# Kernel tuning notes

Measured on AMD Instinct MI355X. Metric: run time of the kernel, lower is better.

## Reference

```python
import jax, jax.numpy as jnp
import numpy as np

HEADS = 8
EPS_LN = 1e-5
EPS_N = 1e-12


def _dw(x, w, b, pad):
    # depthwise conv, NCHW, weight [C,1,kh,kw]
    C = x.shape[1]
    y = jax.lax.conv_general_dilated(x, w, (1, 1), pad,
                                     dimension_numbers=('NCHW', 'OIHW', 'NCHW'),
                                     feature_group_count=C)
    return y + b[None, :, None, None]


def _pw(x, w, b):
    # 1x1 conv as einsum, weight [Cout, Cin]
    return jnp.einsum('bihw,oi->bohw', x, w) + b[None, :, None, None]


def _l2n(x):
    n = jnp.sqrt(jnp.sum(x * x, axis=-1, keepdims=True))
    return x / jnp.maximum(n, EPS_N)


def _axis_attn(q, k, v):
    # q,k,v: [B, heads, N, D]; L2-normalized QK, softmax, +q residual
    q = _l2n(q)
    k = _l2n(k)
    attn = jax.nn.softmax(jnp.einsum('bhnd,bhmd->bhnm', q, k), axis=-1)
    return jnp.einsum('bhnm,bhmd->bhnd', attn, v) + q


def setup_inputs() -> dict:
    key = jax.random.key(0)
    B, C, H, W = 16, 256, 80, 80
    ks = jax.random.split(key, 16)

    def nrm(k, shape, s=0.02):
        return jax.random.normal(k, shape, dtype=jnp.float32) * s

    z = lambda *s: jnp.zeros(s, jnp.float32)
    return {
        'x': nrm(ks[0], (B, C, H, W), 1.0),
        'ln_g': jnp.ones((C,), jnp.float32),
        'ln_b': z(C),
        'w_in': nrm(ks[1], (C, C)), 'b_in': z(C),
        'w_out': nrm(ks[2], (C, C)), 'b_out': z(C),
        'wx7': nrm(ks[3], (C, 1, 1, 7)), 'bx7': z(C),
        'wx11': nrm(ks[4], (C, 1, 1, 11)), 'bx11': z(C),
        'wx21': nrm(ks[5], (C, 1, 1, 21)), 'bx21': z(C),
        'wy7': nrm(ks[6], (C, 1, 7, 1)), 'by7': z(C),
        'wy11': nrm(ks[7], (C, 1, 11, 1)), 'by11': z(C),
        'wy21': nrm(ks[8], (C, 1, 21, 1)), 'by21': z(C),
    }


def reference(x, ln_g, ln_b, w_in, b_in, w_out, b_out,
              wx7, bx7, wx11, bx11, wx21, bx21,
              wy7, by7, wy11, by11, wy21, by21):
    B, C, H, W = x.shape
    cp = C // HEADS

    # LayerNorm over channel dim (applied per-pixel)
    mu = jnp.mean(x, axis=1, keepdims=True)
    var = jnp.var(x, axis=1, keepdims=True)
    xn = (x - mu) / jnp.sqrt(var + EPS_LN)
    xn = xn * ln_g[None, :, None, None] + ln_b[None, :, None, None]

    fx = _pw(_dw(xn, wx7, bx7, ((0, 0), (3, 3)))
             + _dw(xn, wx11, bx11, ((0, 0), (5, 5)))
             + _dw(xn, wx21, bx21, ((0, 0), (10, 10))), w_in, b_in)
    fy = _pw(_dw(xn, wy7, by7, ((3, 3), (0, 0)))
             + _dw(xn, wy11, by11, ((5, 5), (0, 0)))
             + _dw(xn, wy21, by21, ((10, 10), (0, 0))), w_in, b_in)

    def to_h(t):  # [B,C,H,W] -> [B,heads,H,W*cp] (w outer, c inner)
        return t.reshape(B, HEADS, cp, H, W).transpose(0, 1, 3, 4, 2).reshape(B, HEADS, H, W * cp)

    def from_h(t):
        return t.reshape(B, HEADS, H, W, cp).transpose(0, 1, 4, 2, 3).reshape(B, C, H, W)

    def to_w(t):  # [B,C,H,W] -> [B,heads,W,H*cp] (h outer, c inner)
        return t.reshape(B, HEADS, cp, H, W).transpose(0, 1, 4, 3, 2).reshape(B, HEADS, W, H * cp)

    def from_w(t):
        return t.reshape(B, HEADS, W, H, cp).transpose(0, 1, 4, 3, 2).reshape(B, C, H, W)

    out_x = from_h(_axis_attn(to_h(fy), to_h(fx), to_h(fx)))
    out_y = from_w(_axis_attn(to_w(fx), to_w(fy), to_w(fy)))

    return _pw(out_x, w_out, b_out) + _pw(out_y, w_out, b_out) + x
```

## Files before the change

kernel.cpp:

```cpp
#include <hip/hip_runtime.h>

typedef unsigned short u16;
typedef unsigned int   u32;

#define NB  16
#define NC  256
#define NH  80
#define NW  80
#define NHW 6400

typedef short bf16x8 __attribute__((ext_vector_type(8)));
typedef float f32x4  __attribute__((ext_vector_type(4)));

__device__ __forceinline__ float b2f(u16 u) {
  union { u32 i; float f; } c; c.i = ((u32)u) << 16; return c.f;
}
__device__ __forceinline__ u16 f2b(float f) {
  union { float f; u32 i; } c; c.f = f;
  return (u16)((c.i + 0x7FFFu + ((c.i >> 16) & 1u)) >> 16);
}
__device__ __forceinline__ float ldx(const void* p, size_t i, int f32f) {
  return f32f ? ((const float*)p)[i] : b2f(((const u16*)p)[i]);
}
__device__ __forceinline__ int getf(int fh, const int* flagp) {
  return (fh >= 0) ? fh : *flagp;
}

__global__ void probe_init(int* __restrict__ flag) { flag[0] = 0; flag[1] = 0; }

__global__ __launch_bounds__(256) void probe_count(const u16* __restrict__ x,
                                                   int* __restrict__ flag)
{
  __shared__ int cnt[256];
  int base = (blockIdx.x * 256 + threadIdx.x) * 16;
  int c = 0;
  uint4 v0 = *(const uint4*)(x + base);
  uint4 v1 = *(const uint4*)(x + base + 8);
  u32 w[8] = {v0.x, v0.y, v0.z, v0.w, v1.x, v1.y, v1.z, v1.w};
  #pragma unroll
  for (int j = 0; j < 8; j++) {
    if (((w[j] >> 7)  & 0xFFu) == 0xFFu) c++;
    if (((w[j] >> 23) & 0xFFu) == 0xFFu) c++;
  }
  cnt[threadIdx.x] = c; __syncthreads();
  for (int s = 128; s > 0; s >>= 1) {
    if (threadIdx.x < s) cnt[threadIdx.x] += cnt[threadIdx.x + s];
    __syncthreads();
  }
  if (threadIdx.x == 0) atomicAdd(&flag[1], cnt[0]);
}

__global__ void probe_decide(int* __restrict__ flag) {
  flag[0] = (flag[1] > 16) ? 1 : 0;
}

struct CvtArgs { const void* src[18]; int cum[19]; };

__global__ __launch_bounds__(256) void cvt_weights(CvtArgs a, float* __restrict__ dst,
                                                   int fh, const int* __restrict__ flagp)
{
  int f = getf(fh, flagp);
  int i = blockIdx.x * 256 + threadIdx.x;
  int s = 0;
  while (i >= a.cum[s + 1]) s++;
  int j = i - a.cum[s];
  float v = f ? ((const float*)a.src[s])[j] : b2f(((const u16*)a.src[s])[j]);
  if (!(v == v) || fabsf(v) > 1e30f) v = 0.f;
  dst[i] = v;
}

__global__ __launch_bounds__(256) void split_w(const float* __restrict__ w_in,
    const float* __restrict__ w_out, u16* __restrict__ WB)
{
  int i = blockIdx.x * 256 + threadIdx.x;
  int mat = i >> 16, idx = i & 65535;
  float v = (mat ? w_out : w_in)[idx];
  u16 hi = f2b(v);
  u16 lo = f2b(v - b2f(hi));
  WB[mat * 131072 + idx] = hi;
  WB[mat * 131072 + 65536 + idx] = lo;
}

__global__ __launch_bounds__(256) void ln_stats(const void* __restrict__ xsrc,
    size_t xoff, int fh, const int* __restrict__ flagp, float2* __restrict__ stats)
{
  int f = getf(fh, flagp);
  int p = blockIdx.x * 256 + threadIdx.x;
  int bl = p / NHW, hw = p % NHW;
  size_t base = xoff + (size_t)bl * NC * NHW + hw;
  float s1 = 0.f, s2 = 0.f;
  for (int c = 0; c < NC; c++) {
    float v = ldx(xsrc, base + (size_t)c * NHW, f);
    s1 += v; s2 += v * v;
  }
  float mean = s1 * (1.f / 256.f);
  float var  = s2 * (1.f / 256.f) - mean * mean;
  stats[p] = make_float2(mean, rsqrtf(var + 1e-5f));
}

__global__ __launch_bounds__(256) void dw_both(const void* __restrict__ xsrc,
    size_t xoff, int fh, const int* __restrict__ flagp,
    const float2* __restrict__ stats,
    const float* __restrict__ g, const float* __restrict__ bt,
    const float* __restrict__ wx7,  const float* __restrict__ bx7,
    const float* __restrict__ wx11, const float* __restrict__ bx11,
    const float* __restrict__ wx21, const float* __restrict__ bx21,
    const float* __restrict__ wy7,  const float* __restrict__ by7,
    const float* __restrict__ wy11, const float* __restrict__ by11,
    const float* __restrict__ wy21, const float* __restrict__ by21,
    u16* __restrict__ sx, u16* __restrict__ sy)
{
  __shared__ float xn[80][81];
  __shared__ float cwx[21], cwy[21];
  __shared__ float cbx, cby;
  int f = getf(fh, flagp);
  int bc = blockIdx.x;
  int c  = bc & 255;
  int bl = bc >> 8;
  int t = threadIdx.x;
  if (t < 21) {
    float v = wx21[c * 21 + t];
    if (t >= 5 && t <= 15) v += wx11[c * 11 + t - 5];
    if (t >= 7 && t <= 13) v += wx7[c * 7 + t - 7];
    cwx[t] = v;
  } else if (t < 42) {
    int j = t - 21;
    float v = wy21[c * 21 + j];
    if (j >= 5 && j <= 15) v += wy11[c * 11 + j - 5];
    if (j >= 7 && j <= 13) v += wy7[c * 7 + j - 7];
    cwy[j] = v;
  } else if (t == 42) { cbx = bx7[c] + bx11[c] + bx21[c]; }
  else if (t == 43)   { cby = by7[c] + by11[c] + by21[c]; }
  float cg = g[c], cbt = bt[c];
  size_t xrow = xoff + (size_t)bc * NHW;
  const float2* st = stats + (size_t)bl * NHW;
  for (int i = t; i < NHW; i += 256) {
    float v = ldx(xsrc, xrow + i, f);
    float2 s = st[i];
    xn[i / 80][i % 80] = (v - s.x) * s.y * cg + cbt;
  }
  __syncthreads();
  float bxv = cbx, byv = cby;
  size_t obase = (size_t)bc * NHW;
  for (int k = 0; k < 25; k++) {
    int p = t + 256 * k;
    int h = p / 80, w = p % 80;
    float ax = bxv, ay = byv;
    #pragma unroll
    for (int d = -10; d <= 10; d++) {
      int wp = w + d;
      if (wp >= 0 && wp < NW) ax += cwx[d + 10] * xn[h][wp];
      int hp = h + d;
      if (hp >= 0 && hp < NH) ay += cwy[d + 10] * xn[hp][w];
    }
    sx[obase + p] = f2b(ax);
    sy[obase + p] = f2b(ay);
  }
}

template<int FINAL>
__global__ __launch_bounds__(256) void pw_mfma_t(const u16* __restrict__ WB,
    u16* io0, u16* io1, const float* __restrict__ bias,
    void* __restrict__ OutBase, size_t out_off,
    const void* __restrict__ xsrc, size_t xoff,
    int fh, const int* __restrict__ flagp)
{
  __shared__ u16 S[32768];
  u16* InT = S;
  u16* Wp  = S + 16384;
  int bl = blockIdx.y;
  int p0 = blockIdx.x * 64;
  int t  = threadIdx.x;
  int lane = t & 63, wid = t >> 6, lg = lane >> 4, lr = lane & 15;
  u16* io = (FINAL || blockIdx.z == 0) ? io0 : io1;

  {
    int kb = t >> 3, pb = t & 7;
    const u16* src = io + (size_t)bl * NC * NHW + p0 + pb * 8;
    u32 r[8][4];
    #pragma unroll
    for (int i = 0; i < 8; i++) {
      uint4 v = *(const uint4*)(src + (size_t)(kb * 8 + i) * NHW);
      r[i][0] = v.x; r[i][1] = v.y; r[i][2] = v.z; r[i][3] = v.w;
    }
    #pragma unroll
    for (int j = 0; j < 8; j++) {
      u32 w[4];
      #pragma unroll
      for (int m = 0; m < 4; m++) {
        u32 a = r[2 * m][j >> 1], b = r[2 * m + 1][j >> 1];
        w[m] = (j & 1) ? ((a >> 16) | (b & 0xFFFF0000u))
                       : ((a & 0xFFFFu) | (b << 16));
      }
      int p = pb * 8 + j;
      *(uint4*)&InT[p * 256 + ((kb ^ j) * 8)] = make_uint4(w[0], w[1], w[2], w[3]);
    }
  }
  __syncthreads();

  f32x4 acc[4][4];
  #pragma unroll
  for (int m = 0; m < 4; m++)
    #pragma unroll
    for (int n = 0; n < 4; n++)
      acc[m][n] = (f32x4){0.f, 0.f, 0.f, 0.f};

  for (int ch = 0; ch < 8; ch++) {
    #pragma unroll
    for (int rep = 0; rep < 8; rep++) {
      int o = rep * 32 + (t >> 3), sg = t & 7;
      uint4 v = *(const uint4*)(WB + (sg >> 2) * 65536 + o * 256 + ch * 32 + (sg & 3) * 8);
      *(uint4*)&Wp[o * 64 + ((sg ^ (o & 7)) * 8)] = v;
    }
    __syncthreads();
    bf16x8 bfr[4];
    #pragma unroll
    for (int n = 0; n < 4; n++) {
      int px = n * 16 + lr;
      bfr[n] = *(const bf16x8*)&InT[px * 256 + (((ch * 4 + lg) ^ (px & 7)) * 8)];
    }
    #pragma unroll
    for (int m = 0; m < 4; m++) {
      int o = (wid * 4 + m) * 16 + lr;
      bf16x8 ahi = *(const bf16x8*)&Wp[o * 64 + ((lg ^ (o & 7)) * 8)];
      bf16x8 alo = *(const bf16x8*)&Wp[o * 64 + (((4 + lg) ^ (o & 7)) * 8)];
      #pragma unroll
      for (int n = 0; n < 4; n++) {
        acc[m][n] = __builtin_amdgcn_mfma_f32_16x16x32_bf16(ahi, bfr[n], acc[m][n], 0, 0, 0);
        acc[m][n] = __builtin_amdgcn_mfma_f32_16x16x32_bf16(alo, bfr[n], acc[m][n], 0, 0, 0);
      }
    }
    __syncthreads();
  }

  if (FINAL) {
    float* Otf = (float*)S;
    #pragma unroll
    for (int m = 0; m < 4; m++)
      #pragma unroll
      for (int r = 0; r < 4; r++) {
        int o = (wid * 4 + m) * 16 + 4 * lg + r;
        float bv = 2.f * bias[o];
        #pragma unroll
        for (int n = 0; n < 4; n++) {
          int px = n * 16 + lr;
          Otf[o * 64 + (px ^ ((o & 7) * 8))] = acc[m][n][r] + bv;
        }
      }
    __syncthreads();
    int f = getf(fh, flagp);
    size_t gbase = ((size_t)bl * NC + t) * NHW + p0;
    #pragma unroll
    for (int j2 = 0; j2 < 16; j2++) {
      float4 v = *(float4*)&Otf[t * 64 + ((j2 * 4) ^ ((t & 7) * 8))];
      size_t gi = gbase + j2 * 4;
      if (f) {
        const float* xp = (const float*)xsrc + xoff + gi;
        v.x += xp[0]; v.y += xp[1]; v.z += xp[2]; v.w += xp[3];
        *(float4*)((float*)OutBase + out_off + gi) = v;
      } else {
        ushort4 xv = *(const ushort4*)((const u16*)xsrc + xoff + gi);
        ushort4 ov;
        ov.x = f2b(v.x + b2f(xv.x)); ov.y = f2b(v.y + b2f(xv.y));
        ov.z = f2b(v.z + b2f(xv.z)); ov.w = f2b(v.w + b2f(xv.w));
        *(ushort4*)((u16*)OutBase + out_off + gi) = ov;
      }
    }
  } else {
    u16* Ot = S;
    #pragma unroll
    for (int m = 0; m < 4; m++)
      #pragma unroll
      for (int r = 0; r < 4; r++) {
        int o = (wid * 4 + m) * 16 + 4 * lg + r;
        float bv = bias[o];
        #pragma unroll
        for (int n = 0; n < 4; n++) {
          int px = n * 16 + lr;
          Ot[o * 64 + (px ^ ((o & 7) * 8))] = f2b(acc[m][n][r] + bv);
        }
      }
    __syncthreads();
    u16* orow = io + ((size_t)bl * NC + t) * NHW + p0;
    #pragma unroll
    for (int j = 0; j < 8; j++) {
      uint4 v = *(uint4*)&Ot[t * 64 + ((j ^ (t & 7)) * 8)];
      *(uint4*)(orow + j * 8) = v;
    }
  }
  (void)OutBase; (void)out_off; (void)xsrc; (void)xoff; (void)flagp; (void)io1;
}

__global__ __launch_bounds__(256) void transpose_sumsq(const u16* __restrict__ fx,
    const u16* __restrict__ fy, u16* __restrict__ fxT, u16* __restrict__ fyT,
    float* __restrict__ rs_fx, float* __restrict__ rs_fy,
    float* __restrict__ cs_fx, float* __restrict__ cs_fy)
{
  __shared__ u16 tile[80][81];
  int pl = blockIdx.x, ten = blockIdx.y;
  const u16* src = (ten ? fy : fx) + (size_t)pl * NHW;
  u16*       dst = (ten ? fyT : fxT) + (size_t)pl * NHW;
  int t = threadIdx.x;
  for (int i = t; i < NHW; i += 256) tile[i / 80][i % 80] = src[i];
  __syncthreads();
  for (int i = t; i < NHW; i += 256) dst[i] = tile[i % 80][i / 80];
  if (t < 80) {
    float s = 0.f;
    #pragma unroll
    for (int k = 0; k < 80; k++) { float v = b2f(tile[t][k]); s += v * v; }
    (ten ? rs_fy : rs_fx)[pl * 80 + t] = s;
  } else if (t < 160) {
    int w = t - 80; float s = 0.f;
    #pragma unroll
    for (int h = 0; h < 80; h++) { float v = b2f(tile[h][w]); s += v * v; }
    (ten ? cs_fy : cs_fx)[pl * 80 + w] = s;
  }
}

__global__ __launch_bounds__(256) void norm_combine(const float* __restrict__ rs_fx,
    const float* __restrict__ rs_fy, const float* __restrict__ cs_fx,
    const float* __restrict__ cs_fy, float* __restrict__ invn, int Nb)
{
  int t = blockIdx.x * 256 + threadIdx.x;
  int blk = Nb * 640;
  int side = t / blk, r = t % blk;
  int b = r / 640, rem = r % 640, hd = rem / 80, row = rem % 80;
  const float* src = (side == 0) ? rs_fy : (side == 1) ? rs_fx : (side == 2) ? cs_fx : cs_fy;
  size_t base = (size_t)(b * 256 + hd * 32) * 80 + row;
  float s = 0.f;
  #pragma unroll
  for (int ci = 0; ci < 32; ci++) s += src[base + ci * 80];
  invn[t] = 1.f / fmaxf(sqrtf(s), 1e-12f);
}

template<int T0, int NT>
__device__ __forceinline__ void gram_wave(const u16* pa, const u16* pb,
                                          int lg, int lr, f32x4* acc)
{
  constexpr int MLO = T0 / 5;
  #pragma unroll
  for (int ch = 0; ch < 3; ch++) {
    bool tz = (ch == 2) && (lg >= 2);
    int kk = ch * 32 + 8 * lg;
    if (tz) kk = 0;
    bf16x8 af[2], bf[5];
    #pragma unroll
    for (int m = 0; m < 2; m++)
      af[m] = *(const bf16x8*)(pa + ((MLO + m) * 16 + lr) * 80 + kk);
    #pragma unroll
    for (int n = 0; n < 5; n++)
      bf[n] = *(const bf16x8*)(pb + (n * 16 + lr) * 80 + kk);
    if (tz) {
      bf16x8 z = {0, 0, 0, 0, 0, 0, 0, 0};
      af[0] = z; af[1] = z;
    }
    #pragma unroll
    for (int j = 0; j < NT; j++) {
      acc[j] = __builtin_amdgcn_mfma_f32_16x16x32_bf16(
          af[(T0 + j) / 5 - MLO], bf[(T0 + j) % 5], acc[j], 0, 0, 0);
    }
  }
}

template<int T0, int NT>
__device__ __forceinline__ void gram_all(const u16* Ab, const u16* Bb,
                                         int lg, int lr, f32x4* acc)
{
  for (int ci = 0; ci < 32; ci++)
    gram_wave<T0, NT>(Ab + (size_t)ci * NHW, Bb + (size_t)ci * NHW, lg, lr, acc);
}

__global__ __launch_bounds__(256) void gram_softmax_mfma(const u16* __restrict__ fx,
    const u16* __restrict__ fy, const u16* __restrict__ fxT, const u16* __restrict__ fyT,
    const float* __restrict__ invn, u16* __restrict__ Sbuf, int Nb)
{
  __shared__ float At[80][81];
  int hd = blockIdx.x, b = blockIdx.y, axis = blockIdx.z;
  size_t sl0 = (size_t)(b * 256 + hd * 32) * NHW;
  const u16* Ab = (axis ? fxT : fy) + sl0;
  const u16* Bb = (axis ? fyT : fx) + sl0;
  int t = threadIdx.x, lane = t & 63, wid = t >> 6;
  int lg = lane >> 4, lr = lane & 15;
  f32x4 acc0 = {0.f, 0.f, 0.f, 0.f};
  f32x4 acc[7];
  #pragma unroll
  for (int j = 0; j < 7; j++) acc[j] = acc0;
  if      (wid == 0) gram_all<0, 7>(Ab, Bb, lg, lr, acc);
  else if (wid == 1) gram_all<7, 6>(Ab, Bb, lg, lr, acc);
  else if (wid == 2) gram_all<13, 6>(Ab, Bb, lg, lr, acc);
  else               gram_all<19, 6>(Ab, Bb, lg, lr, acc);
  int blk = Nb * 640;
  int rowbase = (b * 8 + hd) * 80;
  const float* invq = invn + (axis ? 2 * blk : 0)   + rowbase;
  const float* invk = invn + (axis ? 3 * blk : blk) + rowbase;
  int t0  = wid ? 6 * wid + 1 : 0;
  int cnt = wid ? 6 : 7;
  #pragma unroll
  for (int j = 0; j < 7; j++) {
    if (j < cnt) {
      int tt = t0 + j, m = tt / 5, n = tt % 5;
      int col = n * 16 + lr;
      float ik = invk[col];
      #pragma unroll
      for (int r = 0; r < 4; r++) {
        int row = m * 16 + 4 * lg + r;
        float gv = acc[j][r] * invq[row] * ik;
        At[row][col] = fminf(fmaxf(gv, -8.f), 8.f);
      }
    }
  }
  __syncthreads();
  u16* Sg = Sbuf + ((size_t)(axis * Nb * 8 + b * 8 + hd)) * NHW;
  if (t < 80) {
    float mx = -1e30f;
    for (int j = 0; j < 80; j++) mx = fmaxf(mx, At[t][j]);
    float s = 0.f;
    for (int j = 0; j < 80; j++) s += __expf(At[t][j] - mx);
    float inv = 1.f / s;
    for (int j = 0; j < 80; j++) Sg[t * 80 + j] = f2b(__expf(At[t][j] - mx) * inv);
  }
}

template<int T0, int NT>
__device__ __forceinline__ void apply_wave(const u16* SH, const u16* fxT,
    const u16* fyP, const u16* SW, int lg, int lr, f32x4* acc)
{
  constexpr int MLO = T0 / 5;
  for (int ch = 0; ch < 3; ch++) {
    bool tz = (ch == 2) && (lg >= 2);
    int kk = ch * 32 + 8 * lg;
    if (tz) kk = 0;
    bf16x8 a1[2], a2[2], b1[5], b2[5];
    #pragma unroll
    for (int m = 0; m < 2; m++) {
      a1[m] = *(const bf16x8*)(SH  + ((MLO + m) * 16 + lr) * 80 + kk);
      a2[m] = *(const bf16x8*)(fyP + ((MLO + m) * 16 + lr) * 80 + kk);
    }
    #pragma unroll
    for (int n = 0; n < 5; n++) {
      b1[n] = *(const bf16x8*)(fxT + (n * 16 + lr) * 80 + kk);
      b2[n] = *(const bf16x8*)(SW  + (n * 16 + lr) * 80 + kk);
    }
    if (tz) {
      bf16x8 z = {0, 0, 0, 0, 0, 0, 0, 0};
      a1[0] = z; a1[1] = z; a2[0] = z; a2[1] = z;
    }
    #pragma unroll
    for (int j = 0; j < NT; j++) {
      acc[j] = __builtin_amdgcn_mfma_f32_16x16x32_bf16(
          a1[(T0 + j) / 5 - MLO], b1[(T0 + j) % 5], acc[j], 0, 0, 0);
      acc[j] = __builtin_amdgcn_mfma_f32_16x16x32_bf16(
          a2[(T0 + j) / 5 - MLO], b2[(T0 + j) % 5], acc[j], 0, 0, 0);
    }
  }
}

__global__ __launch_bounds__(256, 2) void apply_hw_mfma(const u16* __restrict__ fy_g,
    const u16* __restrict__ fxT_g, const u16* __restrict__ Sbuf,
    const float* __restrict__ invn, u16* fx_io, int Nb)
{
  int ci = blockIdx.x, hd = blockIdx.y, b = blockIdx.z;
  size_t off = (size_t)(b * 256 + hd * 32 + ci) * NHW;
  const u16* SgH = Sbuf + (size_t)(b * 8 + hd) * NHW;
  const u16* SgW = Sbuf + ((size_t)(Nb * 8) + b * 8 + hd) * NHW;
  const u16* fyP = fy_g + off;
  const u16* fxT = fxT_g + off;
  int t = threadIdx.x, lane = t & 63, wid = t >> 6;
  int lg = lane >> 4, lr = lane & 15;
  f32x4 acc0 = {0.f, 0.f, 0.f, 0.f};
  f32x4 acc[7];
  #pragma unroll
  for (int j = 0; j < 7; j++) acc[j] = acc0;
  if      (wid == 0) apply_wave<0, 7>(SgH, fxT, fyP, SgW, lg, lr, acc);
  else if (wid == 1) apply_wave<7, 6>(SgH, fxT, fyP, SgW, lg, lr, acc);
  else if (wid == 2) apply_wave<13, 6>(SgH, fxT, fyP, SgW, lg, lr, acc);
  else               apply_wave<19, 6>(SgH, fxT, fyP, SgW, lg, lr, acc);
  const float* invqH = invn + (b * 8 + hd) * 80;
  const float* invqW = invn + 2 * Nb * 640 + (b * 8 + hd) * 80;
  int t0  = wid ? 6 * wid + 1 : 0;
  int cnt = wid ? 6 : 7;
  #pragma unroll
  for (int j = 0; j < 7; j++) {
    if (j < cnt) {
      int tt = t0 + j, m = tt / 5, n = tt % 5;
      int col = n * 16 + lr;
      float ivW = invqW[col];
      #pragma unroll
      for (int r = 0; r < 4; r++) {
        int row = m * 16 + 4 * lg + r;
        size_t ix = off + row * 80 + col;
        float v = acc[j][r] + b2f(fy_g[ix]) * invqH[row] + b2f(fx_io[ix]) * ivW;
        fx_io[ix] = f2b(v);
      }
    }
  }
}

extern "C" void kernel_launch(void* const* d_in, const int* in_sizes, int n_in,
                              void* d_out, int out_size, void* d_ws, size_t ws_size,
                              hipStream_t stream) {
  const int wsz[18] = {256, 256, 65536, 256, 65536, 256,
                       1792, 256, 2816, 256, 5376, 256,
                       1792, 256, 2816, 256, 5376, 256};
  CvtArgs ca;
  int cum = 0;
  for (int i = 0; i < 18; i++) { ca.src[i] = d_in[i + 1]; ca.cum[i] = cum; cum += wsz[i]; }
  ca.cum[18] = cum;

  int hostf = -1;
  if (in_sizes && n_in > 0) {
    if      (in_sizes[0] == 104857600) hostf = 1;
    else if (in_sizes[0] == 52428800)  hostf = 0;
  }
  if (hostf < 0) {
    if      (out_size == 104857600) hostf = 1;
    else if (out_size == 52428800)  hostf = 0;
  }

  int Nb = 1;
  for (int cand = 16; cand >= 1; cand >>= 1) {
    size_t need = (size_t)cand * 13701120 + 614416 + 524288;
    if (need <= ws_size) { Nb = cand; break; }
  }
  char* p = (char*)d_ws;
  int*    flag  = (int*)p;    p += 16;
  float*  wbuf  = (float*)p;  p += 614400;
  u16*    wsplit= (u16*)p;    p += 524288;
  u16*    fxbuf = (u16*)p;    p += (size_t)Nb * 3276800;
  u16*    fybuf = (u16*)p;    p += (size_t)Nb * 3276800;
  u16*    fxT   = (u16*)p;    p += (size_t)Nb * 3276800;
  u16*    fyT   = (u16*)p;    p += (size_t)Nb * 3276800;
  float2* stats = (float2*)p; p += (size_t)Nb * 51200;
  float*  rs_fx = (float*)p;  p += (size_t)Nb * 81920;
  float*  rs_fy = (float*)p;  p += (size_t)Nb * 81920;
  float*  cs_fx = (float*)p;  p += (size_t)Nb * 81920;
  float*  cs_fy = (float*)p;  p += (size_t)Nb * 81920;
  float*  invn  = (float*)p;  p += (size_t)Nb * 10240;
  u16*    Sbuf  = (u16*)p;

  float* ln_g = wbuf + ca.cum[0];  float* ln_b = wbuf + ca.cum[1];
  float* w_in = wbuf + ca.cum[2];  float* b_in = wbuf + ca.cum[3];
  float* w_out= wbuf + ca.cum[4]; float* b_out= wbuf + ca.cum[5];
  float* wx7  = wbuf + ca.cum[6];  float* bx7  = wbuf + ca.cum[7];
  float* wx11 = wbuf + ca.cum[8];  float* bx11 = wbuf + ca.cum[9];
  float* wx21 = wbuf + ca.cum[10]; float* bx21 = wbuf + ca.cum[11];
  float* wy7  = wbuf + ca.cum[12]; float* by7  = wbuf + ca.cum[13];
  float* wy11 = wbuf + ca.cum[14]; float* by11 = wbuf + ca.cum[15];
  float* wy21 = wbuf + ca.cum[16]; float* by21 = wbuf + ca.cum[17];

  if (hostf < 0) {
    probe_init<<<dim3(1), dim3(1), 0, stream>>>(flag);
    probe_count<<<dim3(64), dim3(256), 0, stream>>>((const u16*)d_in[0], flag);
    probe_decide<<<dim3(1), dim3(1), 0, stream>>>(flag);
  }
  cvt_weights<<<dim3(600), dim3(256), 0, stream>>>(ca, wbuf, hostf, flag);
  split_w<<<dim3(512), dim3(256), 0, stream>>>(w_in, w_out, wsplit);

  for (int b0 = 0; b0 < NB; b0 += Nb) {
    size_t xoff = (size_t)b0 * NC * NHW;

    ln_stats<<<dim3(Nb * 25), dim3(256), 0, stream>>>(d_in[0], xoff, hostf, flag, stats);
    dw_both<<<dim3(Nb * 256), dim3(256), 0, stream>>>(d_in[0], xoff, hostf, flag, stats,
        ln_g, ln_b, wx7, bx7, wx11, bx11, wx21, bx21,
        wy7, by7, wy11, by11, wy21, by21, fxbuf, fybuf);
    pw_mfma_t<0><<<dim3(100, Nb, 2), dim3(256), 0, stream>>>(wsplit, fxbuf, fybuf,
        b_in, nullptr, 0, nullptr, 0, hostf, flag);
    transpose_sumsq<<<dim3(Nb * 256, 2), dim3(256), 0, stream>>>(fxbuf, fybuf, fxT, fyT,
        rs_fx, rs_fy, cs_fx, cs_fy);
    norm_combine<<<dim3(10 * Nb), dim3(256), 0, stream>>>(rs_fx, rs_fy, cs_fx, cs_fy, invn, Nb);
    gram_softmax_mfma<<<dim3(8, Nb, 2), dim3(256), 0, stream>>>(fxbuf, fybuf, fxT, fyT, invn, Sbuf, Nb);
    apply_hw_mfma<<<dim3(32, 8, Nb), dim3(256), 0, stream>>>(fybuf, fxT, Sbuf, invn, fxbuf, Nb);
    pw_mfma_t<1><<<dim3(100, Nb, 1), dim3(256), 0, stream>>>(wsplit + 131072, fxbuf, nullptr,
        b_out, d_out, xoff, d_in[0], xoff, hostf, flag);
  }
  (void)in_sizes; (void)n_in; (void)out_size;
}
```

Before: 953.4 us.

## Vectorize LN stats loads and register-block depthwise convs with padded smem

```diff
diff --git a/kernel.cpp b/kernel.cpp
--- a/kernel.cpp
+++ b/kernel.cpp
@@ -85,17 +85,38 @@
     size_t xoff, int fh, const int* __restrict__ flagp, float2* __restrict__ stats)
 {
   int f = getf(fh, flagp);
-  int p = blockIdx.x * 256 + threadIdx.x;
-  int bl = p / NHW, hw = p % NHW;
-  size_t base = xoff + (size_t)bl * NC * NHW + hw;
-  float s1 = 0.f, s2 = 0.f;
-  for (int c = 0; c < NC; c++) {
-    float v = ldx(xsrc, base + (size_t)c * NHW, f);
-    s1 += v; s2 += v * v;
-  }
-  float mean = s1 * (1.f / 256.f);
-  float var  = s2 * (1.f / 256.f) - mean * mean;
-  stats[p] = make_float2(mean, rsqrtf(var + 1e-5f));
+  int bl = blockIdx.y;
+  int p4 = blockIdx.x * 1024 + threadIdx.x * 4;
+  if (p4 >= NHW) return;
+  size_t base = xoff + (size_t)bl * NC * NHW + p4;
+  float s1[4] = {0.f, 0.f, 0.f, 0.f}, s2[4] = {0.f, 0.f, 0.f, 0.f};
+  if (f) {
+    const float* xp = (const float*)xsrc + base;
+    for (int c = 0; c < NC; c++) {
+      float4 v = *(const float4*)(xp + (size_t)c * NHW);
+      s1[0] += v.x; s2[0] += v.x * v.x;
+      s1[1] += v.y; s2[1] += v.y * v.y;
+      s1[2] += v.z; s2[2] += v.z * v.z;
+      s1[3] += v.w; s2[3] += v.w * v.w;
+    }
+  } else {
+    const u16* xp = (const u16*)xsrc + base;
+    for (int c = 0; c < NC; c++) {
+      ushort4 v = *(const ushort4*)(xp + (size_t)c * NHW);
+      float a = b2f(v.x), b = b2f(v.y), cc = b2f(v.z), d = b2f(v.w);
+      s1[0] += a;  s2[0] += a * a;
+      s1[1] += b;  s2[1] += b * b;
+      s1[2] += cc; s2[2] += cc * cc;
+      s1[3] += d;  s2[3] += d * d;
+    }
+  }
+  float2* so = stats + (size_t)bl * NHW + p4;
+  #pragma unroll
+  for (int j = 0; j < 4; j++) {
+    float mean = s1[j] * (1.f / 256.f);
+    float var  = s2[j] * (1.f / 256.f) - mean * mean;
+    so[j] = make_float2(mean, rsqrtf(var + 1e-5f));
+  }
 }
 
 __global__ __launch_bounds__(256) void dw_both(const void* __restrict__ xsrc,
@@ -110,9 +131,9 @@
     const float* __restrict__ wy21, const float* __restrict__ by21,
     u16* __restrict__ sx, u16* __restrict__ sy)
 {
-  __shared__ float xn[80][81];
+  __shared__ float xnp[80][116];
   __shared__ float cwx[21], cwy[21];
-  __shared__ float cbx, cby;
+  __shared__ float cbs[2];
   int f = getf(fh, flagp);
   int bc = blockIdx.x;
   int c  = bc & 255;
@@ -129,32 +150,58 @@
     if (j >= 5 && j <= 15) v += wy11[c * 11 + j - 5];
     if (j >= 7 && j <= 13) v += wy7[c * 7 + j - 7];
     cwy[j] = v;
-  } else if (t == 42) { cbx = bx7[c] + bx11[c] + bx21[c]; }
-  else if (t == 43)   { cby = by7[c] + by11[c] + by21[c]; }
+  } else if (t == 42) { cbs[0] = bx7[c] + bx11[c] + bx21[c]; }
+  else if (t == 43)   { cbs[1] = by7[c] + by11[c] + by21[c]; }
+  for (int i = t; i < 2560; i += 256) {
+    int rr = i >> 5, cc = i & 31;
+    xnp[rr][cc < 16 ? cc : 80 + cc] = 0.f;
+  }
   float cg = g[c], cbt = bt[c];
   size_t xrow = xoff + (size_t)bc * NHW;
   const float2* st = stats + (size_t)bl * NHW;
   for (int i = t; i < NHW; i += 256) {
     float v = ldx(xsrc, xrow + i, f);
     float2 s = st[i];
-    xn[i / 80][i % 80] = (v - s.x) * s.y * cg + cbt;
+    xnp[i / 80][16 + i % 80] = (v - s.x) * s.y * cg + cbt;
   }
   __syncthreads();
-  float bxv = cbx, byv = cby;
+  float bxv = cbs[0], byv = cbs[1];
   size_t obase = (size_t)bc * NHW;
-  for (int k = 0; k < 25; k++) {
-    int p = t + 256 * k;
-    int h = p / 80, w = p % 80;
-    float ax = bxv, ay = byv;
-    #pragma unroll
-    for (int d = -10; d <= 10; d++) {
-      int wp = w + d;
-      if (wp >= 0 && wp < NW) ax += cwx[d + 10] * xn[h][wp];
-      int hp = h + d;
-      if (hp >= 0 && hp < NH) ay += cwy[d + 10] * xn[hp][w];
-    }
-    sx[obase + p] = f2b(ax);
-    sy[obase + p] = f2b(ay);
+  for (int u = t; u < 800; u += 256) {
+    int h = u / 10, w0 = (u % 10) * 8;
+    float r[32];
+    #pragma unroll
+    for (int j = 0; j < 8; j++)
+      *(float4*)&r[4 * j] = *(const float4*)&xnp[h][w0 + 4 + 4 * j];
+    float ax[8], ay[8];
+    #pragma unroll
+    for (int j = 0; j < 8; j++) { ax[j] = bxv; ay[j] = byv; }
+    #pragma unroll
+    for (int dd = 0; dd < 21; dd++) {
+      float wv = cwx[dd];
+      #pragma unroll
+      for (int j = 0; j < 8; j++) ax[j] += wv * r[j + 2 + dd];
+    }
+    #pragma unroll
+    for (int dd = 0; dd < 21; dd++) {
+      int hp = h + dd - 10;
+      int hc = min(max(hp, 0), 79);
+      float wv = (hp == hc) ? cwy[dd] : 0.f;
+      float4 v0 = *(const float4*)&xnp[hc][16 + w0];
+      float4 v1 = *(const float4*)&xnp[hc][20 + w0];
+      ay[0] += wv * v0.x; ay[1] += wv * v0.y; ay[2] += wv * v0.z; ay[3] += wv * v0.w;
+      ay[4] += wv * v1.x; ay[5] += wv * v1.y; ay[6] += wv * v1.z; ay[7] += wv * v1.w;
+    }
+    size_t ob = obase + h * 80 + w0;
+    ushort4 a0, a1, b0, b1;
+    a0.x = f2b(ax[0]); a0.y = f2b(ax[1]); a0.z = f2b(ax[2]); a0.w = f2b(ax[3]);
+    a1.x = f2b(ax[4]); a1.y = f2b(ax[5]); a1.z = f2b(ax[6]); a1.w = f2b(ax[7]);
+    b0.x = f2b(ay[0]); b0.y = f2b(ay[1]); b0.z = f2b(ay[2]); b0.w = f2b(ay[3]);
+    b1.x = f2b(ay[4]); b1.y = f2b(ay[5]); b1.z = f2b(ay[6]); b1.w = f2b(ay[7]);
+    *(ushort4*)(sx + ob)     = a0;
+    *(ushort4*)(sx + ob + 4) = a1;
+    *(ushort4*)(sy + ob)     = b0;
+    *(ushort4*)(sy + ob + 4) = b1;
   }
 }
 
@@ -559,7 +606,7 @@
   for (int b0 = 0; b0 < NB; b0 += Nb) {
     size_t xoff = (size_t)b0 * NC * NHW;
 
-    ln_stats<<<dim3(Nb * 25), dim3(256), 0, stream>>>(d_in[0], xoff, hostf, flag, stats);
+    ln_stats<<<dim3(7, Nb), dim3(256), 0, stream>>>(d_in[0], xoff, hostf, flag, stats);
     dw_both<<<dim3(Nb * 256), dim3(256), 0, stream>>>(d_in[0], xoff, hostf, flag, stats,
         ln_g, ln_b, wx7, bx7, wx11, bx11, wx21, bx21,
         wy7, by7, wy11, by11, wy21, by21, fxbuf, fybuf);
```

After: 860.3 us. 1.11x faster.
